# Kernel tuning notes

Hardware: AMD Instinct MI355X
Metric: run time of the kernel (lower is better)

The kernel has to match this reference:

```python
import jax, jax.numpy as jnp
import numpy as np

NS, NT, DIN, DOUT = 4096, 8192, 256, 128


def setup_inputs() -> dict:
    key = jax.random.key(0)
    k1, k2, k3, k4, k5, k6 = jax.random.split(key, 6)
    inp_s = jax.random.normal(k1, (NS, DIN), dtype=jnp.float32)
    inp_t = jax.random.normal(k2, (NT, DIN), dtype=jnp.float32)
    # nonnegative adjacency weights (original graphs have 0/1 entries)
    adj = jax.random.uniform(k3, (NS, NT), dtype=jnp.float32)
    adj_s = jax.random.uniform(k4, (NS, NS), dtype=jnp.float32)
    adj_t = jax.random.uniform(k5, (NT, NT), dtype=jnp.float32)
    init_range = np.sqrt(6.0 / (DIN + DOUT))
    W = jax.random.uniform(k6, (DIN, DOUT), minval=-init_range, maxval=init_range,
                           dtype=jnp.float32)
    return {"inp_s": inp_s, "inp_t": inp_t, "adj": adj, "adj_s": adj_s,
            "adj_t": adj_t, "W": W}


def reference(inp_s, inp_t, adj, adj_s, adj_t, W):
    # project both node sets with shared weights (dropout = 0.0)
    x = inp_s @ W                                   # [Ns, Dout]
    y = inp_t @ W                                   # [Nt, Dout]

    # degree normalization (add-one before sqrt)
    deg_so = jnp.sum(adj, axis=1, keepdims=True) + jnp.sum(adj_s, axis=1, keepdims=True)  # [Ns,1]
    root_deg_so = jnp.sqrt(deg_so + 1.0)            # [Ns,1]
    deg_to = jnp.sum(adj, axis=0, keepdims=True) + jnp.sum(adj_t, axis=0, keepdims=True)  # [1,Nt]
    root_deg_to = jnp.sqrt(deg_to + 1.0)            # [1,Nt]

    nrm_adj_s = adj_s / root_deg_so / root_deg_so.T  # [Ns,Ns]
    nrm_adj_t = adj_t / root_deg_to / root_deg_to.T  # [Nt,Nt]
    nrm_adj = adj / root_deg_so / root_deg_to        # [Ns,Nt]

    x = jax.nn.relu(x / root_deg_so + nrm_adj_s @ x + nrm_adj @ y)
    # note: updated (activated) x feeds into y's cross term, as in the original
    y = jax.nn.relu(y / root_deg_to.T + nrm_adj_t @ y + nrm_adj.T @ x)
    return (x, y)
```

## Files before the change

kernel.cpp:

```cpp
#include <hip/hip_runtime.h>

#define NS 4096
#define NT 8192
#define DIN 256
#define DOUT 128

#define OFF_RS   0
#define OFF_RT   (NS)
#define OFF_C1   (OFF_RT + NT)
#define OFF_C2   (OFF_C1 + NS*DOUT)
#define OFF_XS   (OFF_C2 + NT*DOUT)
#define OFF_YS   (OFF_XS + NS*DOUT)
#define OFF_XNS  (OFF_YS + NT*DOUT)
#define OFF_XST  (OFF_XNS + NS*DOUT)
#define OFF_YST  (OFF_XST + (128*NS)/2)

typedef __attribute__((ext_vector_type(8))) short bf8v;
typedef __attribute__((ext_vector_type(4))) float f32x4;
typedef __attribute__((ext_vector_type(4))) unsigned short u16x4;

__device__ __forceinline__ ushort f2bf(float f) {
    unsigned x = __float_as_uint(f);
    unsigned r = (x + 0x7fffu + ((x >> 16) & 1u)) >> 16;
    return (ushort)r;
}

__global__ void zero_kernel(float* __restrict__ p, int n4) {
    int i = blockIdx.x * blockDim.x + threadIdx.x;
    int stride = gridDim.x * blockDim.x;
    float4* p4 = (float4*)p;
    float4 z = make_float4(0.f, 0.f, 0.f, 0.f);
    for (; i < n4; i += stride) p4[i] = z;
}

__global__ __launch_bounds__(256)
void adj_deg_kernel(const float* __restrict__ adj,
                    float* __restrict__ deg_s, float* __restrict__ deg_t) {
    const int tid = threadIdx.x;
    const int lane = tid & 63;
    const int c4 = blockIdx.x * 256 + tid;
    const int r0 = blockIdx.y * 32;
    const float4* A4 = (const float4*)adj + (size_t)r0 * (NT / 4) + c4;
    float sx = 0.f, sy = 0.f, sz = 0.f, sw = 0.f;
#pragma unroll 8
    for (int r = 0; r < 32; ++r) {
        float4 v = A4[(size_t)r * (NT / 4)];
        sx += v.x; sy += v.y; sz += v.z; sw += v.w;
        float rp = v.x + v.y + v.z + v.w;
#pragma unroll
        for (int off = 32; off > 0; off >>= 1) rp += __shfl_down(rp, off, 64);
        if (lane == 0) unsafeAtomicAdd(deg_s + r0 + r, rp);
    }
    float* d = deg_t + c4 * 4;
    unsafeAtomicAdd(d + 0, sx);
    unsafeAtomicAdd(d + 1, sy);
    unsafeAtomicAdd(d + 2, sz);
    unsafeAtomicAdd(d + 3, sw);
}

__global__ __launch_bounds__(256)
void rowsum_s_kernel(const float* __restrict__ adj_s, float* __restrict__ deg_s) {
    const int wid = threadIdx.x >> 6;
    const int lane = threadIdx.x & 63;
    const int row = blockIdx.x * 4 + wid;
    const float4* b = (const float4*)(adj_s + (size_t)row * NS);
    float sum = 0.f;
#pragma unroll 8
    for (int c = lane; c < NS / 4; c += 64) { float4 v = b[c]; sum += v.x + v.y + v.z + v.w; }
#pragma unroll
    for (int off = 32; off > 0; off >>= 1) sum += __shfl_down(sum, off, 64);
    if (lane == 0) unsafeAtomicAdd(deg_s + row, sum);
}

__global__ __launch_bounds__(256)
void colsum_t_kernel(const float* __restrict__ A, float* __restrict__ deg_t) {
    const int c4 = blockIdx.x * 256 + threadIdx.x;
    const int r0 = blockIdx.y * 64;
    const float4* A4 = (const float4*)A + (size_t)r0 * (NT / 4) + c4;
    float sx = 0.f, sy = 0.f, sz = 0.f, sw = 0.f;
#pragma unroll 8
    for (int r = 0; r < 64; ++r) {
        float4 v = A4[(size_t)r * (NT / 4)];
        sx += v.x; sy += v.y; sz += v.z; sw += v.w;
    }
    float* d = deg_t + c4 * 4;
    unsafeAtomicAdd(d + 0, sx);
    unsafeAtomicAdd(d + 1, sy);
    unsafeAtomicAdd(d + 2, sz);
    unsafeAtomicAdd(d + 3, sw);
}

__global__ void finish_deg_kernel(float* __restrict__ deg) {
    int t = blockIdx.x * blockDim.x + threadIdx.x;
    deg[t] = sqrtf(deg[t] + 1.0f);
}

__global__ __launch_bounds__(256)
void proj_scale_kernel(const float* __restrict__ inp,
                       const float* __restrict__ W,
                       const float* __restrict__ rdeg,
                       float* __restrict__ outp,
                       ushort* __restrict__ outT, int M) {
    __shared__ float As[32][68];
    __shared__ float Bs[32][128];
    const int tid = threadIdx.x;
    const int m0 = blockIdx.x * 64;
    const int tx = tid & 15, ty = tid >> 4;
    const int arow = tid >> 3, acg = tid & 7;
    const int bk = tid >> 5, bng = tid & 31;

    float acc[4][8];
#pragma unroll
    for (int r = 0; r < 4; ++r)
#pragma unroll
        for (int c = 0; c < 8; ++c) acc[r][c] = 0.f;

    for (int kt = 0; kt < DIN; kt += 32) {
        const float* Ab = inp + (size_t)(m0 + arow) * DIN + kt + acg * 4;
        float4 a0 = *(const float4*)Ab;
        float4 a1 = *(const float4*)(Ab + (size_t)32 * DIN);
        const float* Bb = W + (size_t)(kt + bk) * DOUT + bng * 4;
        float4 b0 = *(const float4*)Bb;
        float4 b1 = *(const float4*)(Bb + 8 * DOUT);
        float4 b2 = *(const float4*)(Bb + 16 * DOUT);
        float4 b3 = *(const float4*)(Bb + 24 * DOUT);
        __syncthreads();
        As[acg * 4 + 0][arow] = a0.x;
        As[acg * 4 + 1][arow] = a0.y;
        As[acg * 4 + 2][arow] = a0.z;
        As[acg * 4 + 3][arow] = a0.w;
        As[acg * 4 + 0][arow + 32] = a1.x;
        As[acg * 4 + 1][arow + 32] = a1.y;
        As[acg * 4 + 2][arow + 32] = a1.z;
        As[acg * 4 + 3][arow + 32] = a1.w;
        *(float4*)&Bs[bk][bng * 4] = b0;
        *(float4*)&Bs[bk + 8][bng * 4] = b1;
        *(float4*)&Bs[bk + 16][bng * 4] = b2;
        *(float4*)&Bs[bk + 24][bng * 4] = b3;
        __syncthreads();
#pragma unroll
        for (int k = 0; k < 32; ++k) {
            float4 av = *(const float4*)&As[k][ty * 4];
            float4 bv0 = *(const float4*)&Bs[k][tx * 4];
            float4 bv1 = *(const float4*)&Bs[k][tx * 4 + 64];
            float a[4] = {av.x, av.y, av.z, av.w};
            float b[8] = {bv0.x, bv0.y, bv0.z, bv0.w, bv1.x, bv1.y, bv1.z, bv1.w};
#pragma unroll
            for (int r = 0; r < 4; ++r)
#pragma unroll
                for (int c = 0; c < 8; ++c) acc[r][c] = fmaf(a[r], b[c], acc[r][c]);
        }
    }
    float rds[4];
#pragma unroll
    for (int r = 0; r < 4; ++r) rds[r] = rdeg[m0 + ty * 4 + r];
#pragma unroll
    for (int r = 0; r < 4; ++r) {
        int row = m0 + ty * 4 + r;
        float* orow = outp + (size_t)row * DOUT;
#pragma unroll
        for (int c = 0; c < 8; ++c) acc[r][c] /= rds[r];
#pragma unroll
        for (int c = 0; c < 4; ++c) {
            orow[tx * 4 + c] = acc[r][c];
            orow[tx * 4 + 64 + c] = acc[r][4 + c];
        }
    }
#pragma unroll
    for (int c = 0; c < 8; ++c) {
        int col = tx * 4 + (c & 3) + (c >> 2) * 64;
        u16x4 w;
#pragma unroll
        for (int r = 0; r < 4; ++r) w[r] = f2bf(acc[r][c]);
        *(u16x4*)&outT[(size_t)col * M + m0 + ty * 4] = w;
    }
}

template<int TRANS, int BTF>
__device__ __forceinline__
void gemm_body(ushort (*As)[40], ushort (*Bs)[40],
               const float* __restrict__ A, int lda,
               const float* __restrict__ Bf,
               const ushort* __restrict__ bT, int ldb,
               float* __restrict__ C, int kchunk, int k0, int m0) {
    const int tid = threadIdx.x;
    const int lane = tid & 63, wid = tid >> 6;
    const int wm = (wid >> 1) * 64, wn = (wid & 1) * 64;
    const int r16 = lane & 15, kg = lane >> 4;

    const int s_kr = tid >> 3, s_f4 = tid & 7;
    const int a_r = tid >> 1, a_seg = tid & 1;
    const int t_n = tid >> 2, t_seg = tid & 3;

    f32x4 acc[4][4];
#pragma unroll
    for (int i = 0; i < 4; ++i)
#pragma unroll
        for (int j = 0; j < 4; ++j) acc[i][j] = (f32x4)(0.f);

    float4 aP[4], bP[4];
    bf8v bPT[2];

    auto loadB = [&](int ktb) {
        if (BTF) {
            const ushort* Tb = bT + (size_t)t_n * ldb + k0 + ktb + t_seg * 8;
            bPT[0] = *(const bf8v*)Tb;
            bPT[1] = *(const bf8v*)(Tb + (size_t)64 * ldb);
        } else {
            const float* Bb = Bf + (size_t)(k0 + ktb + s_kr) * DOUT + s_f4 * 4;
#pragma unroll
            for (int i = 0; i < 4; ++i) bP[i] = *(const float4*)(Bb + i * 32);
        }
    };
    auto loadA = [&](int ktb) {
        if (TRANS) {
            const float* Ab = A + (size_t)(k0 + ktb + s_kr) * lda + m0 + s_f4 * 4;
#pragma unroll
            for (int i = 0; i < 4; ++i) aP[i] = *(const float4*)(Ab + i * 32);
        } else {
            const float* Ab = A + (size_t)(m0 + a_r) * lda + k0 + ktb + a_seg * 16;
#pragma unroll
            for (int i = 0; i < 4; ++i) aP[i] = *(const float4*)(Ab + i * 4);
        }
    };

    loadB(0); loadA(0);

    for (int kt = 0; kt < kchunk; kt += 32) {
        __syncthreads();
        if (TRANS) {
#pragma unroll
            for (int i = 0; i < 4; ++i) {
                int m = s_f4 * 4 + i * 32;
                As[m + 0][s_kr] = f2bf(aP[i].x);
                As[m + 1][s_kr] = f2bf(aP[i].y);
                As[m + 2][s_kr] = f2bf(aP[i].z);
                As[m + 3][s_kr] = f2bf(aP[i].w);
            }
        } else {
            bf8v w0, w1;
            w0[0] = (short)f2bf(aP[0].x); w0[1] = (short)f2bf(aP[0].y);
            w0[2] = (short)f2bf(aP[0].z); w0[3] = (short)f2bf(aP[0].w);
            w0[4] = (short)f2bf(aP[1].x); w0[5] = (short)f2bf(aP[1].y);
            w0[6] = (short)f2bf(aP[1].z); w0[7] = (short)f2bf(aP[1].w);
            w1[0] = (short)f2bf(aP[2].x); w1[1] = (short)f2bf(aP[2].y);
            w1[2] = (short)f2bf(aP[2].z); w1[3] = (short)f2bf(aP[2].w);
            w1[4] = (short)f2bf(aP[3].x); w1[5] = (short)f2bf(aP[3].y);
            w1[6] = (short)f2bf(aP[3].z); w1[7] = (short)f2bf(aP[3].w);
            *(bf8v*)&As[a_r][a_seg * 16] = w0;
            *(bf8v*)&As[a_r][a_seg * 16 + 8] = w1;
        }
        if (BTF) {
            *(bf8v*)&Bs[t_n][t_seg * 8] = bPT[0];
            *(bf8v*)&Bs[t_n + 64][t_seg * 8] = bPT[1];
        } else {
#pragma unroll
            for (int i = 0; i < 4; ++i) {
                int n = s_f4 * 4 + i * 32;
                Bs[n + 0][s_kr] = f2bf(bP[i].x);
                Bs[n + 1][s_kr] = f2bf(bP[i].y);
                Bs[n + 2][s_kr] = f2bf(bP[i].z);
                Bs[n + 3][s_kr] = f2bf(bP[i].w);
            }
        }
        __syncthreads();

        if (kt + 32 < kchunk) { loadB(kt + 32); loadA(kt + 32); }

        bf8v af[4], bfv[4];
#pragma unroll
        for (int f = 0; f < 4; ++f) af[f] = *(const bf8v*)&As[wm + f * 16 + r16][kg * 8];
#pragma unroll
        for (int f = 0; f < 4; ++f) bfv[f] = *(const bf8v*)&Bs[wn + f * 16 + r16][kg * 8];
#pragma unroll
        for (int i = 0; i < 4; ++i)
#pragma unroll
            for (int j = 0; j < 4; ++j)
                acc[i][j] = __builtin_amdgcn_mfma_f32_16x16x32_bf16(af[i], bfv[j], acc[i][j], 0, 0, 0);
    }

    const int crow0 = m0 + wm + (lane >> 4) * 4;
#pragma unroll
    for (int i = 0; i < 4; ++i) {
#pragma unroll
        for (int j = 0; j < 4; ++j) {
            float* base = C + (size_t)(crow0 + i * 16) * DOUT + wn + j * 16 + r16;
            unsafeAtomicAdd(base + 0 * DOUT, acc[i][j][0]);
            unsafeAtomicAdd(base + 1 * DOUT, acc[i][j][1]);
            unsafeAtomicAdd(base + 2 * DOUT, acc[i][j][2]);
            unsafeAtomicAdd(base + 3 * DOUT, acc[i][j][3]);
        }
    }
}

template<int TRANS0, int BTF0, int TRANS1, int BTF1>
__global__ __launch_bounds__(256)
void gemm_dual_kernel(const float* __restrict__ A0, int lda0,
                      const float* __restrict__ B0f, const ushort* __restrict__ B0T, int ldb0,
                      int kchunk0, int nsplit0,
                      const float* __restrict__ A1, int lda1,
                      const float* __restrict__ B1f, const ushort* __restrict__ B1T, int ldb1,
                      int kchunk1,
                      float* __restrict__ C) {
    __shared__ ushort As[128][40];
    __shared__ ushort Bs[128][40];
    const int m0 = blockIdx.x * 128;
    const int y = blockIdx.y;
    if (y < nsplit0) {
        gemm_body<TRANS0, BTF0>(As, Bs, A0, lda0, B0f, B0T, ldb0, C, kchunk0, y * kchunk0, m0);
    } else {
        gemm_body<TRANS1, BTF1>(As, Bs, A1, lda1, B1f, B1T, ldb1, C, kchunk1, (y - nsplit0) * kchunk1, m0);
    }
}

__global__ void epilogue1_kernel(const float* __restrict__ C1,
                                 const float* __restrict__ xs,
                                 const float* __restrict__ rs,
                                 float* __restrict__ outx,
                                 float* __restrict__ xns) {
    int idx = blockIdx.x * blockDim.x + threadIdx.x;
    if (idx >= NS * DOUT) return;
    int row = idx >> 7;
    float r = rs[row];
    float v = xs[idx] + C1[idx] / r;
    v = v > 0.f ? v : 0.f;
    outx[idx] = v;
    xns[idx] = v / r;
}

__global__ void epilogue2_kernel(const float* __restrict__ C2,
                                 const float* __restrict__ ys,
                                 const float* __restrict__ rt,
                                 float* __restrict__ outy) {
    int idx = blockIdx.x * blockDim.x + threadIdx.x;
    if (idx >= NT * DOUT) return;
    int row = idx >> 7;
    float v = ys[idx] + C2[idx] / rt[row];
    v = v > 0.f ? v : 0.f;
    outy[idx] = v;
}

extern "C" void kernel_launch(void* const* d_in, const int* in_sizes, int n_in,
                              void* d_out, int out_size, void* d_ws, size_t ws_size,
                              hipStream_t stream) {
    const float* inp_s = (const float*)d_in[0];
    const float* inp_t = (const float*)d_in[1];
    const float* adj   = (const float*)d_in[2];
    const float* adj_s = (const float*)d_in[3];
    const float* adj_t = (const float*)d_in[4];
    const float* W     = (const float*)d_in[5];
    float* out = (float*)d_out;
    float* ws  = (float*)d_ws;

    float* rs  = ws + OFF_RS;
    float* rt  = ws + OFF_RT;
    float* C1  = ws + OFF_C1;
    float* C2  = ws + OFF_C2;
    float* xs  = ws + OFF_XS;
    float* ys  = ws + OFF_YS;
    float* xns = ws + OFF_XNS;
    ushort* xsT = (ushort*)(ws + OFF_XST);
    ushort* ysT = (ushort*)(ws + OFF_YST);

    zero_kernel<<<1024, 256, 0, stream>>>(ws, OFF_XS / 4);

    colsum_t_kernel<<<dim3(NT / 1024, NT / 64), 256, 0, stream>>>(adj_t, rt);
    adj_deg_kernel<<<dim3(NT / 1024, NS / 32), 256, 0, stream>>>(adj, rs, rt);
    rowsum_s_kernel<<<NS / 4, 256, 0, stream>>>(adj_s, rs);
    finish_deg_kernel<<<(NS + NT) / 256, 256, 0, stream>>>(rs);

    proj_scale_kernel<<<NS / 64, 256, 0, stream>>>(inp_s, W, rs, xs, xsT, NS);
    proj_scale_kernel<<<NT / 64, 256, 0, stream>>>(inp_t, W, rt, ys, ysT, NT);

    gemm_dual_kernel<0, 1, 0, 1><<<dim3(NS / 128, 16), 256, 0, stream>>>(
        adj_s, NS, nullptr, xsT, NS, NS / 8, 8,
        adj,   NT, nullptr, ysT, NT, NT / 8, C1);
    epilogue1_kernel<<<(NS * DOUT) / 256, 256, 0, stream>>>(C1, xs, rs, out, xns);

    gemm_dual_kernel<1, 0, 0, 1><<<dim3(NT / 128, 16), 256, 0, stream>>>(
        adj,   NT, xns, nullptr, 0, NS / 8, 8,
        adj_t, NT, nullptr, ysT, NT, NT / 8, C2);
    epilogue2_kernel<<<(NT * DOUT) / 256, 256, 0, stream>>>(C2, ys, rt, out + NS * DOUT);
}
```

Before: 360.9 us.

## Move independent adj_t@y GEMM into first launch alongside x-side GEMMs

The adj_t @ y product does not depend on the updated x, so it is moved out of the second dual GEMM and into a new triple-GEMM launch with the adj_s@x and adj@y products, using a flattened 1D grid. The second launch then only computes adj^T @ xns. This balances work across the two dependent phases and gives the first launch more blocks to fill the GPU. The cost is a larger first launch and a smaller, possibly under-occupied second one.

New measurement: 352.9 us. -2.2%, faster.

```diff
diff --git a/kernel.cpp b/kernel.cpp
--- a/kernel.cpp
+++ b/kernel.cpp
@@ -293,24 +293,33 @@
     }
 }
 
-template<int TRANS0, int BTF0, int TRANS1, int BTF1>
-__global__ __launch_bounds__(256)
-void gemm_dual_kernel(const float* __restrict__ A0, int lda0,
-                      const float* __restrict__ B0f, const ushort* __restrict__ B0T, int ldb0,
-                      int kchunk0, int nsplit0,
-                      const float* __restrict__ A1, int lda1,
-                      const float* __restrict__ B1f, const ushort* __restrict__ B1T, int ldb1,
-                      int kchunk1,
-                      float* __restrict__ C) {
+__global__ __launch_bounds__(256)
+void gemm_triple_kernel(const float* __restrict__ A0, int lda0, const ushort* __restrict__ B0T, int ldb0, int kc0, int n0,
+                        const float* __restrict__ A1, int lda1, const ushort* __restrict__ B1T, int ldb1, int kc1, int n1,
+                        const float* __restrict__ A2, int lda2, const ushort* __restrict__ B2T, int ldb2, int kc2,
+                        float* __restrict__ C0, float* __restrict__ C2) {
     __shared__ ushort As[128][40];
     __shared__ ushort Bs[128][40];
-    const int m0 = blockIdx.x * 128;
-    const int y = blockIdx.y;
-    if (y < nsplit0) {
-        gemm_body<TRANS0, BTF0>(As, Bs, A0, lda0, B0f, B0T, ldb0, C, kchunk0, y * kchunk0, m0);
+    int bid = blockIdx.x;
+    if (bid < n0) {
+        gemm_body<0, 1>(As, Bs, A0, lda0, nullptr, B0T, ldb0, C0, kc0, (bid & 7) * kc0, (bid >> 3) * 128);
+    } else if (bid < n0 + n1) {
+        int b = bid - n0;
+        gemm_body<0, 1>(As, Bs, A1, lda1, nullptr, B1T, ldb1, C0, kc1, (b & 7) * kc1, (b >> 3) * 128);
     } else {
-        gemm_body<TRANS1, BTF1>(As, Bs, A1, lda1, B1f, B1T, ldb1, C, kchunk1, (y - nsplit0) * kchunk1, m0);
-    }
+        int b = bid - n0 - n1;
+        gemm_body<0, 1>(As, Bs, A2, lda2, nullptr, B2T, ldb2, C2, kc2, (b & 7) * kc2, (b >> 3) * 128);
+    }
+}
+
+template<int TRANS, int BTF>
+__global__ __launch_bounds__(256)
+void gemm_single_kernel(const float* __restrict__ A, int lda,
+                        const float* __restrict__ Bf, const ushort* __restrict__ bT, int ldb,
+                        float* __restrict__ C, int kchunk) {
+    __shared__ ushort As[128][40];
+    __shared__ ushort Bs[128][40];
+    gemm_body<TRANS, BTF>(As, Bs, A, lda, Bf, bT, ldb, C, kchunk, blockIdx.y * kchunk, blockIdx.x * 128);
 }
 
 __global__ void epilogue1_kernel(const float* __restrict__ C1,
@@ -372,13 +381,13 @@
     proj_scale_kernel<<<NS / 64, 256, 0, stream>>>(inp_s, W, rs, xs, xsT, NS);
     proj_scale_kernel<<<NT / 64, 256, 0, stream>>>(inp_t, W, rt, ys, ysT, NT);
 
-    gemm_dual_kernel<0, 1, 0, 1><<<dim3(NS / 128, 16), 256, 0, stream>>>(
-        adj_s, NS, nullptr, xsT, NS, NS / 8, 8,
-        adj,   NT, nullptr, ysT, NT, NT / 8, C1);
+    gemm_triple_kernel<<<1024, 256, 0, stream>>>(
+        adj_s, NS, xsT, NS, NS / 8, 256,
+        adj,   NT, ysT, NT, NT / 8, 256,
+        adj_t, NT, ysT, NT, NT / 8,
+        C1, C2);
     epilogue1_kernel<<<(NS * DOUT) / 256, 256, 0, stream>>>(C1, xs, rs, out, xns);
 
-    gemm_dual_kernel<1, 0, 0, 1><<<dim3(NT / 128, 16), 256, 0, stream>>>(
-        adj,   NT, xns, nullptr, 0, NS / 8, 8,
-        adj_t, NT, nullptr, ysT, NT, NT / 8, C2);
+    gemm_single_kernel<1, 0><<<dim3(NT / 128, 8), 256, 0, stream>>>(adj, NT, xns, nullptr, 0, C2, NS / 8);
     epilogue2_kernel<<<(NT * DOUT) / 256, 256, 0, stream>>>(C2, ys, rt, out + NS * DOUT);
 }
```
